# Optimization experiments

Hardware: AMD Instinct MI355X
Metric: run time of the kernel (lower is better)

## Reference

```python
import jax, jax.numpy as jnp
import numpy as np

HIDDEN = 256
EDGE_DIM = 16
HEADS = 8
HEAD_DIM = HIDDEN // HEADS
B, N = 4, 512


def setup_inputs() -> dict:
    key = jax.random.key(0)
    ks = jax.random.split(key, 16)
    s = 1.0 / np.sqrt(HIDDEN)
    se = 1.0 / np.sqrt(EDGE_DIM)
    return {
        "node_h": jax.random.normal(ks[0], (B, N, HIDDEN), jnp.float32),
        "edge_x": jax.random.normal(ks[1], (B, N, N, EDGE_DIM), jnp.float32),
        "edge_mask": jax.random.randint(ks[2], (B, N, N), 0, 2, jnp.int32),
        "Wq": jax.random.normal(ks[3], (HIDDEN, HIDDEN), jnp.float32) * s,
        "bq": jnp.zeros((HIDDEN,), jnp.float32),
        "Wk": jax.random.normal(ks[4], (HIDDEN, HIDDEN), jnp.float32) * s,
        "bk": jnp.zeros((HIDDEN,), jnp.float32),
        "Wv": jax.random.normal(ks[5], (HIDDEN, HIDDEN), jnp.float32) * s,
        "bv": jnp.zeros((HIDDEN,), jnp.float32),
        "We1": jax.random.normal(ks[6], (EDGE_DIM, HIDDEN), jnp.float32) * se,
        "be1": jnp.zeros((HIDDEN,), jnp.float32),
        "We2": jax.random.normal(ks[7], (HIDDEN, HEADS), jnp.float32) * s,
        "be2": jnp.zeros((HEADS,), jnp.float32),
        "Wo": jax.random.normal(ks[8], (HIDDEN, HIDDEN), jnp.float32) * s,
        "bo": jnp.zeros((HIDDEN,), jnp.float32),
        "ln_g": jnp.ones((HIDDEN,), jnp.float32),
        "ln_b": jnp.zeros((HIDDEN,), jnp.float32),
    }


def reference(node_h, edge_x, edge_mask, Wq, bq, Wk, bk, Wv, bv,
              We1, be1, We2, be2, Wo, bo, ln_g, ln_b):
    Bsz, Nn, _ = node_h.shape
    # projections -> [B, H, N, D]
    def heads(x):
        return x.reshape(Bsz, Nn, HEADS, HEAD_DIM).transpose(0, 2, 1, 3)
    q = heads(node_h @ Wq + bq)
    k = heads(node_h @ Wk + bk)
    v = heads(node_h @ Wv + bv)

    scores = jnp.einsum('bhid,bhjd->bhij', q, k) / np.sqrt(HEAD_DIM)
    scores = jax.nn.leaky_relu(scores, negative_slope=0.2)

    # edge bias MLP: [B,N,N,E] -> [B,N,N,H] -> [B,H,N,N]
    eb = jax.nn.relu(edge_x @ We1 + be1) @ We2 + be2
    scores = scores + eb.transpose(0, 3, 1, 2)

    valid = (edge_mask != 0) | jnp.eye(Nn, dtype=bool)[None]  # [B,N,N]
    scores = jnp.where(valid[:, None], scores, -1e9)

    attn = jax.nn.softmax(scores, axis=-1)
    out = jnp.einsum('bhij,bhjd->bhid', attn, v)
    out = out.transpose(0, 2, 1, 3).reshape(Bsz, Nn, HIDDEN)
    out = out @ Wo + bo

    x = node_h + out
    mu = jnp.mean(x, axis=-1, keepdims=True)
    var = jnp.var(x, axis=-1, keepdims=True)
    x = (x - mu) / jnp.sqrt(var + 1e-5) * ln_g + ln_b
    return jax.nn.relu(x), attn
```

## Files before the change

kernel.cpp:

```cpp
#include <hip/hip_runtime.h>

#define BATCH 4
#define NN 512
#define HID 256
#define EDIM 16
#define HEADS 8
#define HDIM 32

typedef __attribute__((ext_vector_type(8))) short bf16x8;
typedef __attribute__((ext_vector_type(4))) float f32x4;

__device__ inline unsigned short bf16_hi(float x){ return (unsigned short)(__float_as_uint(x)>>16); }
__device__ inline float bf16_f(unsigned short s){ return __uint_as_float(((unsigned)s)<<16); }
__device__ inline unsigned short bf16_rn(float x){
    unsigned u = __float_as_uint(x);
    unsigned r = u + 0x7FFFu + ((u>>16)&1u);
    return (unsigned short)(r>>16);
}
__device__ inline unsigned cvt_pk_bf16(float a, float b){
    unsigned d;
    asm("v_cvt_pk_bf16_f32 %0, %1, %2" : "=v"(d) : "v"(a), "v"(b));
    return d;
}
__device__ inline void hilo8(float4 A, float4 B, bf16x8& hi, bf16x8& lo){
    float xs[8] = {A.x,A.y,A.z,A.w,B.x,B.y,B.z,B.w};
    unsigned hu[4], lu[4];
#pragma unroll
    for (int p = 0; p < 4; ++p){
        unsigned u0 = __float_as_uint(xs[2*p]), u1 = __float_as_uint(xs[2*p+1]);
        float h0 = __uint_as_float(u0 & 0xFFFF0000u);
        float h1 = __uint_as_float(u1 & 0xFFFF0000u);
        hu[p] = (u0 >> 16) | (u1 & 0xFFFF0000u);
        lu[p] = cvt_pk_bf16(xs[2*p] - h0, xs[2*p+1] - h1);
    }
    int4 hv; hv.x = hu[0]; hv.y = hu[1]; hv.z = hu[2]; hv.w = hu[3];
    int4 lv; lv.x = lu[0]; lv.y = lu[1]; lv.z = lu[2]; lv.w = lu[3];
    hi = *(bf16x8*)&hv; lo = *(bf16x8*)&lv;
}

__global__ void k_pack(const float* __restrict__ We1, const float* __restrict__ be1,
                       const float* __restrict__ We2,
                       unsigned short* __restrict__ W1P, unsigned short* __restrict__ W2P) {
    int t = threadIdx.x;
#pragma unroll
    for (int rep = 0; rep < 4; ++rep) {
        int p = rep * 256 + t;
        int ut = p >> 6, lane = p & 63;
        int q = lane >> 4, r = lane & 15;
        int unit = ut * 16 + r;
#pragma unroll
        for (int j = 0; j < 8; ++j) {
            int k = q * 8 + j;
            unsigned short ov;
            if (k < 16) ov = bf16_hi(We1[k * HID + unit]);
            else if (k < 31) {
                float v = We1[(k - 16) * HID + unit];
                ov = bf16_rn(v - bf16_f(bf16_hi(v)));
            } else ov = bf16_rn(be1[unit]);
            W1P[p * 8 + j] = ov;
        }
    }
#pragma unroll
    for (int rep = 0; rep < 2; ++rep) {
        int p = rep * 256 + t;
        int kt = p >> 6, lane = p & 63;
        int q = lane >> 4, r = lane & 15;
#pragma unroll
        for (int jj = 0; jj < 8; ++jj) {
            int unit = kt * 32 + q * 8 + jj;
            W2P[p * 8 + jj] = (r < 8) ? bf16_rn(We2[unit * HEADS + r]) : (unsigned short)0;
        }
    }
}

__global__ __launch_bounds__(256) void k_qkv(
    const float* __restrict__ node_h,
    const float* __restrict__ Wq, const float* __restrict__ bq,
    const float* __restrict__ Wk, const float* __restrict__ bk,
    const float* __restrict__ Wv, const float* __restrict__ bv,
    float* __restrict__ q, float* __restrict__ k, float* __restrict__ vT) {
    int blk = blockIdx.x;
    int b = blk >> 7, i0 = (blk & 127) << 2;
    int t = threadIdx.x;
    __shared__ __align__(16) float s_h[4][HID];
#pragma unroll
    for (int u = 0; u < 4; ++u)
        s_h[u][t] = node_h[((size_t)b * NN + i0 + u) * HID + t];
    __syncthreads();
    float aq[4], ak[4], av[4];
    float bqv = bq[t], bkv = bk[t], bvv = bv[t];
#pragma unroll
    for (int u = 0; u < 4; ++u) { aq[u] = bqv; ak[u] = bkv; av[u] = bvv; }
#pragma unroll 4
    for (int rr = 0; rr < HID; ++rr) {
        float wq = Wq[rr * HID + t], wk = Wk[rr * HID + t], wv = Wv[rr * HID + t];
#pragma unroll
        for (int u = 0; u < 4; ++u) {
            float x = s_h[u][rr];
            aq[u] = fmaf(x, wq, aq[u]);
            ak[u] = fmaf(x, wk, ak[u]);
            av[u] = fmaf(x, wv, av[u]);
        }
    }
    int h = t >> 5, d = t & 31;
#pragma unroll
    for (int u = 0; u < 4; ++u) {
        size_t idx = ((size_t)(b * HEADS + h) * NN + i0 + u) * HDIM + d;
        q[idx] = aq[u]; k[idx] = ak[u];
        vT[((size_t)(b * HEADS + h) * HDIM + d) * NN + i0 + u] = av[u];
    }
}

__global__ __launch_bounds__(256, 3) void k_eb(
    const float* __restrict__ edge_x,
    const unsigned short* __restrict__ W1P, const unsigned short* __restrict__ W2P,
    const float* __restrict__ be2, float* __restrict__ eb) {
    int bid = blockIdx.x;
    int b = bid >> 9, i0 = ((bid >> 2) & 127) << 2, jq = bid & 3;
    int t = threadIdx.x;
    int w = t >> 6, lane = t & 63;
    int q2 = lane >> 4, r = lane & 15;

    __shared__ __align__(16) unsigned short sW1[8192];
    __shared__ __align__(16) unsigned short sW2[4096];

    {
        const float4* s1 = (const float4*)W1P;
        float4* d1 = (float4*)sW1;
#pragma unroll
        for (int rep = 0; rep < 4; ++rep) d1[rep * 256 + t] = s1[rep * 256 + t];
        const float4* s2 = (const float4*)W2P;
        float4* d2 = (float4*)sW2;
#pragma unroll
        for (int rep = 0; rep < 2; ++rep) d2[rep * 256 + t] = s2[rep * 256 + t];
    }
    __syncthreads();

    float be2r = (r < 8) ? be2[r] : 0.f;
    const char* wb1 = (const char*)sW1 + lane * 16;
    const char* wb2 = (const char*)sW2 + lane * 16;

    size_t xbase = (((size_t)b * NN + i0 + w) * NN) * EDIM + (size_t)((q2 & 1) * 8);
    const f32x4 zero4 = {0.f, 0.f, 0.f, 0.f};

    for (int sc = 0; sc < 2; ++sc) {
        int cc0 = jq * 8 + sc * 4;
        float4 xv[8];
#pragma unroll
        for (int x = 0; x < 4; ++x) {
            const float4* px = (const float4*)(edge_x + xbase + (size_t)((cc0 + x) * 16 + r) * EDIM);
            xv[2 * x]     = px[0];
            xv[2 * x + 1] = px[1];
        }
        bf16x8 bx[4];
#pragma unroll
        for (int x = 0; x < 4; ++x) {
            unsigned u0 = cvt_pk_bf16(xv[2*x].x, xv[2*x].y);
            unsigned u1 = cvt_pk_bf16(xv[2*x].z, xv[2*x].w);
            unsigned u2 = cvt_pk_bf16(xv[2*x+1].x, xv[2*x+1].y);
            unsigned u3 = cvt_pk_bf16(xv[2*x+1].z, xv[2*x+1].w);
            if (q2 == 3) u3 = (u3 & 0xFFFFu) | 0x3F800000u;
            int4 bxi; bxi.x = u0; bxi.y = u1; bxi.z = u2; bxi.w = u3;
            bx[x] = *(bf16x8*)&bxi;
        }
        f32x4 acc0[4], acc1[4];
#pragma unroll
        for (int x = 0; x < 4; ++x) {
            acc0[x] = (f32x4){be2r, be2r, be2r, be2r};
            acc1[x] = zero4;
        }
#pragma unroll
        for (int ktp = 0; ktp < 8; ++ktp) {
            bf16x8 wa = *(const bf16x8*)(wb1 + (2 * ktp) * 1024);
            bf16x8 wb = *(const bf16x8*)(wb1 + (2 * ktp + 1) * 1024);
            bf16x8 w2 = *(const bf16x8*)(wb2 + ktp * 1024);
#pragma unroll
            for (int x = 0; x < 4; ++x) {
                f32x4 c0 = __builtin_amdgcn_mfma_f32_16x16x32_bf16(wa, bx[x], zero4, 0, 0, 0);
                f32x4 c1 = __builtin_amdgcn_mfma_f32_16x16x32_bf16(wb, bx[x], zero4, 0, 0, 0);
                unsigned P0 = cvt_pk_bf16(fmaxf(c0[0], 0.f), fmaxf(c0[1], 0.f));
                unsigned P1 = cvt_pk_bf16(fmaxf(c0[2], 0.f), fmaxf(c0[3], 0.f));
                unsigned Q0 = cvt_pk_bf16(fmaxf(c1[0], 0.f), fmaxf(c1[1], 0.f));
                unsigned Q1 = cvt_pk_bf16(fmaxf(c1[2], 0.f), fmaxf(c1[3], 0.f));
                asm("v_permlane32_swap_b32 %0, %1" : "+v"(P0), "+v"(Q0));
                asm("v_permlane16_swap_b32 %0, %1" : "+v"(P0), "+v"(Q0));
                asm("v_permlane32_swap_b32 %0, %1" : "+v"(P1), "+v"(Q1));
                asm("v_permlane16_swap_b32 %0, %1" : "+v"(P1), "+v"(Q1));
                int4 ai; ai.x = (int)P0; ai.y = (int)P1; ai.z = (int)Q0; ai.w = (int)Q1;
                if (ktp & 1)
                    acc1[x] = __builtin_amdgcn_mfma_f32_16x16x32_bf16(*(bf16x8*)&ai, w2, acc1[x], 0, 0, 0);
                else
                    acc0[x] = __builtin_amdgcn_mfma_f32_16x16x32_bf16(*(bf16x8*)&ai, w2, acc0[x], 0, 0, 0);
            }
        }
        if (r < 8) {
#pragma unroll
            for (int x = 0; x < 4; ++x) {
                f32x4 a = acc0[x] + acc1[x];
                *(f32x4*)(eb + (((size_t)(b * HEADS + r) * NN) + (i0 + w)) * NN + (cc0 + x) * 16 + q2 * 4) = a;
            }
        }
    }
}

__global__ __launch_bounds__(256, 3) void k_attn2(
    const int* __restrict__ emask,
    const float* __restrict__ q, const float* __restrict__ k, const float* __restrict__ vT,
    float* attn, float* __restrict__ ao) {
    int bid = blockIdx.x;
    int b = bid >> 8, h = (bid >> 5) & 7, ic = bid & 31;
    int i0 = ic << 4;
    int t = threadIdx.x, w = t >> 6, lane = t & 63;
    int q2 = lane >> 4, r = lane & 15;
    size_t bh = (size_t)b * HEADS + h;

    __shared__ __align__(16) float s_sc[16][516];
    __shared__ __align__(16) unsigned short s_ab[16][520];
    __shared__ float s_out[2][16][33];

    bf16x8 qhi, qlo;
    {
        const float4* qp = (const float4*)(q + ((bh * NN) + i0 + r) * HDIM + q2 * 8);
        hilo8(qp[0], qp[1], qhi, qlo);
    }

    const float scale = 0.17677669529663687f;
    for (int c = 0; c < 8; ++c) {
        int jt = w * 8 + c;
        bf16x8 khi, klo;
        {
            const float4* kp = (const float4*)(k + (bh * NN + jt * 16 + r) * HDIM + q2 * 8);
            hilo8(kp[0], kp[1], khi, klo);
        }
        f32x4 cc = {0.f, 0.f, 0.f, 0.f};
        cc = __builtin_amdgcn_mfma_f32_16x16x32_bf16(qhi, khi, cc, 0, 0, 0);
        cc = __builtin_amdgcn_mfma_f32_16x16x32_bf16(qhi, klo, cc, 0, 0, 0);
        cc = __builtin_amdgcn_mfma_f32_16x16x32_bf16(qlo, khi, cc, 0, 0, 0);
        int j = jt * 16 + r;
#pragma unroll
        for (int reg = 0; reg < 4; ++reg) {
            int row = q2 * 4 + reg;
            int i = i0 + row;
            float s = cc[reg] * scale;
            s = s > 0.f ? s : 0.2f * s;
            s += attn[(bh * NN + i) * NN + j];
            bool valid = (emask[((size_t)b * NN + i) * NN + j] != 0) || (j == i);
            s_sc[row][j] = valid ? s : -1e9f;
        }
    }
    __syncthreads();

#pragma unroll
    for (int rr = 0; rr < 4; ++rr) {
        int row = w * 4 + rr;
        f32x4 v0 = *(f32x4*)&s_sc[row][lane * 8];
        f32x4 v1 = *(f32x4*)&s_sc[row][lane * 8 + 4];
        float mx = fmaxf(fmaxf(fmaxf(v0[0], v0[1]), fmaxf(v0[2], v0[3])),
                         fmaxf(fmaxf(v1[0], v1[1]), fmaxf(v1[2], v1[3])));
#pragma unroll
        for (int off = 32; off > 0; off >>= 1) mx = fmaxf(mx, __shfl_xor(mx, off));
        float e[8];
        e[0] = __expf(v0[0] - mx); e[1] = __expf(v0[1] - mx);
        e[2] = __expf(v0[2] - mx); e[3] = __expf(v0[3] - mx);
        e[4] = __expf(v1[0] - mx); e[5] = __expf(v1[1] - mx);
        e[6] = __expf(v1[2] - mx); e[7] = __expf(v1[3] - mx);
        float sum = ((e[0] + e[1]) + (e[2] + e[3])) + ((e[4] + e[5]) + (e[6] + e[7]));
#pragma unroll
        for (int off = 32; off > 0; off >>= 1) sum += __shfl_xor(sum, off);
        float inv = 1.f / sum;
#pragma unroll
        for (int l = 0; l < 8; ++l) e[l] *= inv;
        float* arow = attn + (bh * NN + i0 + row) * NN + lane * 8;
        float4 o0; o0.x = e[0]; o0.y = e[1]; o0.z = e[2]; o0.w = e[3];
        float4 o1; o1.x = e[4]; o1.y = e[5]; o1.z = e[6]; o1.w = e[7];
        *(float4*)(arow) = o0;
        *(float4*)(arow + 4) = o1;
        uint4 pk;
        pk.x = cvt_pk_bf16(e[0], e[1]); pk.y = cvt_pk_bf16(e[2], e[3]);
        pk.z = cvt_pk_bf16(e[4], e[5]); pk.w = cvt_pk_bf16(e[6], e[7]);
        *(uint4*)((char*)s_ab + row * 1040 + lane * 16) = pk;
    }
    __syncthreads();

    {
        int part = w >> 1, nh = w & 1;
        const float* vbase = vT + (bh * HDIM + nh * 16 + r) * NN;
        f32x4 acc = {0.f, 0.f, 0.f, 0.f};
        for (int kt = 0; kt < 16; ++kt) {
            bf16x8 af = *(bf16x8*)((char*)s_ab + r * 1040 + kt * 64 + q2 * 16);
            const float4* vp = (const float4*)(vbase + kt * 32 + q2 * 8);
            float4 x0 = vp[0], x1 = vp[1];
            float xs[8] = {x0.x, x0.y, x0.z, x0.w, x1.x, x1.y, x1.z, x1.w};
            bf16x8 bfg;
            if (part == 0) {
                unsigned hu[4];
#pragma unroll
                for (int p = 0; p < 4; ++p) {
                    unsigned a0 = __float_as_uint(xs[2*p]), a1 = __float_as_uint(xs[2*p+1]);
                    hu[p] = (a0 >> 16) | (a1 & 0xFFFF0000u);
                }
                int4 hv; hv.x = hu[0]; hv.y = hu[1]; hv.z = hu[2]; hv.w = hu[3];
                bfg = *(bf16x8*)&hv;
            } else {
                unsigned lu[4];
#pragma unroll
                for (int p = 0; p < 4; ++p) {
                    unsigned a0 = __float_as_uint(xs[2*p]), a1 = __float_as_uint(xs[2*p+1]);
                    float h0 = __uint_as_float(a0 & 0xFFFF0000u);
                    float h1 = __uint_as_float(a1 & 0xFFFF0000u);
                    lu[p] = cvt_pk_bf16(xs[2*p] - h0, xs[2*p+1] - h1);
                }
                int4 lv; lv.x = lu[0]; lv.y = lu[1]; lv.z = lu[2]; lv.w = lu[3];
                bfg = *(bf16x8*)&lv;
            }
            acc = __builtin_amdgcn_mfma_f32_16x16x32_bf16(af, bfg, acc, 0, 0, 0);
        }
#pragma unroll
        for (int reg = 0; reg < 4; ++reg)
            s_out[part][q2 * 4 + reg][nh * 16 + r] = acc[reg];
    }
    __syncthreads();

#pragma unroll
    for (int rep = 0; rep < 2; ++rep) {
        int idx = rep * 256 + t;
        int row = idx >> 5, d = idx & 31;
        ao[((size_t)b * NN + i0 + row) * HID + h * HDIM + d] =
            s_out[0][row][d] + s_out[1][row][d];
    }
}

__global__ __launch_bounds__(256) void k_final(
    const float* __restrict__ ao, const float* __restrict__ node_h,
    const float* __restrict__ Wo, const float* __restrict__ bo,
    const float* __restrict__ ln_g, const float* __restrict__ ln_b,
    float* __restrict__ out) {
    int blk = blockIdx.x;
    size_t bi0 = (size_t)blk * 4;
    int t = threadIdx.x;
    __shared__ __align__(16) float s_a[4][HID];
    __shared__ float s_red[4][4][2];
#pragma unroll
    for (int u = 0; u < 4; ++u)
        s_a[u][t] = ao[(bi0 + u) * HID + t];
    __syncthreads();
    float bov = bo[t];
    float o[4];
#pragma unroll
    for (int u = 0; u < 4; ++u) o[u] = bov;
#pragma unroll 4
    for (int rr = 0; rr < HID; ++rr) {
        float wo = Wo[rr * HID + t];
#pragma unroll
        for (int u = 0; u < 4; ++u) o[u] = fmaf(s_a[u][rr], wo, o[u]);
    }
    float g = ln_g[t], bb = ln_b[t];
    int wave = t >> 6, ln = t & 63;
    float x[4];
#pragma unroll
    for (int u = 0; u < 4; ++u) {
        x[u] = node_h[(bi0 + u) * HID + t] + o[u];
        float s1 = x[u], s2 = x[u] * x[u];
#pragma unroll
        for (int off = 32; off > 0; off >>= 1) { s1 += __shfl_xor(s1, off); s2 += __shfl_xor(s2, off); }
        if (ln == 0) { s_red[u][wave][0] = s1; s_red[u][wave][1] = s2; }
    }
    __syncthreads();
#pragma unroll
    for (int u = 0; u < 4; ++u) {
        float s1 = s_red[u][0][0] + s_red[u][1][0] + s_red[u][2][0] + s_red[u][3][0];
        float s2 = s_red[u][0][1] + s_red[u][1][1] + s_red[u][2][1] + s_red[u][3][1];
        float mean = s1 * (1.f / HID);
        float var = s2 * (1.f / HID) - mean * mean;
        float inv = rsqrtf(var + 1e-5f);
        float y = (x[u] - mean) * inv * g + bb;
        out[(bi0 + u) * HID + t] = fmaxf(y, 0.f);
    }
}

extern "C" void kernel_launch(void* const* d_in, const int* in_sizes, int n_in,
                              void* d_out, int out_size, void* d_ws, size_t ws_size,
                              hipStream_t stream) {
    const float* node_h = (const float*)d_in[0];
    const float* edge_x = (const float*)d_in[1];
    const int*   emask  = (const int*)d_in[2];
    const float* Wq = (const float*)d_in[3];
    const float* bq = (const float*)d_in[4];
    const float* Wk = (const float*)d_in[5];
    const float* bk = (const float*)d_in[6];
    const float* Wv = (const float*)d_in[7];
    const float* bv = (const float*)d_in[8];
    const float* We1 = (const float*)d_in[9];
    const float* be1 = (const float*)d_in[10];
    const float* We2 = (const float*)d_in[11];
    const float* be2 = (const float*)d_in[12];
    const float* Wo = (const float*)d_in[13];
    const float* bo = (const float*)d_in[14];
    const float* ln_g = (const float*)d_in[15];
    const float* ln_b = (const float*)d_in[16];

    float* out_x  = (float*)d_out;
    float* out_at = (float*)d_out + (size_t)BATCH * NN * HID;

    float* ws = (float*)d_ws;
    float* q    = ws;
    float* kbuf = ws + 524288;
    float* vT   = ws + 1048576;
    float* ao   = ws + 1572864;
    unsigned short* W1P = (unsigned short*)(ws + 2097152);
    unsigned short* W2P = W1P + 8192;

    const int NBI = BATCH * NN;

    hipLaunchKernelGGL(k_pack, dim3(1), dim3(256), 0, stream, We1, be1, We2, W1P, W2P);
    hipLaunchKernelGGL(k_qkv, dim3(NBI / 4), dim3(256), 0, stream,
                       node_h, Wq, bq, Wk, bk, Wv, bv, q, kbuf, vT);
    hipLaunchKernelGGL(k_eb, dim3(2048), dim3(256), 0, stream,
                       edge_x, W1P, W2P, be2, out_at);
    hipLaunchKernelGGL(k_attn2, dim3(1024), dim3(256), 0, stream,
                       emask, q, kbuf, vT, out_at, ao);
    hipLaunchKernelGGL(k_final, dim3(NBI / 4), dim3(256), 0, stream,
                       ao, node_h, Wo, bo, ln_g, ln_b, out_x);
}
```

Baseline: 147.6 us.

## Precompute bf16 hi/lo splits of K and V in projection kernel

The QKV projection kernel now writes K and V as separate bf16 hi and lo arrays, so the attention kernel no longer converts fp32 to bf16 in its inner loops. The attention kernel loads the bf16 fragments directly, which halves K/V read traffic per MFMA pass and drops the V conversion ALU work. It also reuses the score shared-memory buffer for the packed probabilities and raises the occupancy hint from 3 to 4 blocks. The cost is extra scattered 2-byte stores in k_qkv, and the aliasing of s_sc relies on the barrier between the softmax and PV phases.

Result: faster. 138.9 us (-5.9%).

```diff
diff --git a/kernel.cpp b/kernel.cpp
--- a/kernel.cpp
+++ b/kernel.cpp
@@ -78,7 +78,9 @@
     const float* __restrict__ Wq, const float* __restrict__ bq,
     const float* __restrict__ Wk, const float* __restrict__ bk,
     const float* __restrict__ Wv, const float* __restrict__ bv,
-    float* __restrict__ q, float* __restrict__ k, float* __restrict__ vT) {
+    float* __restrict__ q,
+    unsigned short* __restrict__ khi, unsigned short* __restrict__ klo,
+    unsigned short* __restrict__ vhi, unsigned short* __restrict__ vlo) {
     int blk = blockIdx.x;
     int b = blk >> 7, i0 = (blk & 127) << 2;
     int t = threadIdx.x;
@@ -106,8 +108,14 @@
 #pragma unroll
     for (int u = 0; u < 4; ++u) {
         size_t idx = ((size_t)(b * HEADS + h) * NN + i0 + u) * HDIM + d;
-        q[idx] = aq[u]; k[idx] = ak[u];
-        vT[((size_t)(b * HEADS + h) * HDIM + d) * NN + i0 + u] = av[u];
+        q[idx] = aq[u];
+        unsigned short kh = bf16_hi(ak[u]);
+        khi[idx] = kh;
+        klo[idx] = bf16_rn(ak[u] - bf16_f(kh));
+        size_t vidx = ((size_t)(b * HEADS + h) * HDIM + d) * NN + i0 + u;
+        unsigned short vh = bf16_hi(av[u]);
+        vhi[vidx] = vh;
+        vlo[vidx] = bf16_rn(av[u] - bf16_f(vh));
     }
 }
 
@@ -203,9 +211,10 @@
     }
 }
 
-__global__ __launch_bounds__(256, 3) void k_attn2(
-    const int* __restrict__ emask,
-    const float* __restrict__ q, const float* __restrict__ k, const float* __restrict__ vT,
+__global__ __launch_bounds__(256, 4) void k_attn2(
+    const int* __restrict__ emask, const float* __restrict__ q,
+    const unsigned short* __restrict__ khi, const unsigned short* __restrict__ klo,
+    const unsigned short* __restrict__ vhi, const unsigned short* __restrict__ vlo,
     float* attn, float* __restrict__ ao) {
     int bid = blockIdx.x;
     int b = bid >> 8, h = (bid >> 5) & 7, ic = bid & 31;
@@ -215,8 +224,8 @@
     size_t bh = (size_t)b * HEADS + h;
 
     __shared__ __align__(16) float s_sc[16][516];
-    __shared__ __align__(16) unsigned short s_ab[16][520];
     __shared__ float s_out[2][16][33];
+    char* sab = (char*)&s_sc[0][0];
 
     bf16x8 qhi, qlo;
     {
@@ -227,15 +236,13 @@
     const float scale = 0.17677669529663687f;
     for (int c = 0; c < 8; ++c) {
         int jt = w * 8 + c;
-        bf16x8 khi, klo;
-        {
-            const float4* kp = (const float4*)(k + (bh * NN + jt * 16 + r) * HDIM + q2 * 8);
-            hilo8(kp[0], kp[1], khi, klo);
-        }
+        size_t kidx = (bh * NN + jt * 16 + r) * HDIM + q2 * 8;
+        bf16x8 kh8 = *(const bf16x8*)(khi + kidx);
+        bf16x8 kl8 = *(const bf16x8*)(klo + kidx);
         f32x4 cc = {0.f, 0.f, 0.f, 0.f};
-        cc = __builtin_amdgcn_mfma_f32_16x16x32_bf16(qhi, khi, cc, 0, 0, 0);
-        cc = __builtin_amdgcn_mfma_f32_16x16x32_bf16(qhi, klo, cc, 0, 0, 0);
-        cc = __builtin_amdgcn_mfma_f32_16x16x32_bf16(qlo, khi, cc, 0, 0, 0);
+        cc = __builtin_amdgcn_mfma_f32_16x16x32_bf16(qhi, kh8, cc, 0, 0, 0);
+        cc = __builtin_amdgcn_mfma_f32_16x16x32_bf16(qhi, kl8, cc, 0, 0, 0);
+        cc = __builtin_amdgcn_mfma_f32_16x16x32_bf16(qlo, kh8, cc, 0, 0, 0);
         int j = jt * 16 + r;
 #pragma unroll
         for (int reg = 0; reg < 4; ++reg) {
@@ -278,41 +285,17 @@
         uint4 pk;
         pk.x = cvt_pk_bf16(e[0], e[1]); pk.y = cvt_pk_bf16(e[2], e[3]);
         pk.z = cvt_pk_bf16(e[4], e[5]); pk.w = cvt_pk_bf16(e[6], e[7]);
-        *(uint4*)((char*)s_ab + row * 1040 + lane * 16) = pk;
+        *(uint4*)(sab + row * 2064 + lane * 16) = pk;
     }
     __syncthreads();
 
     {
         int part = w >> 1, nh = w & 1;
-        const float* vbase = vT + (bh * HDIM + nh * 16 + r) * NN;
+        const unsigned short* vbase = (part == 0 ? vhi : vlo) + (bh * HDIM + nh * 16 + r) * NN;
         f32x4 acc = {0.f, 0.f, 0.f, 0.f};
         for (int kt = 0; kt < 16; ++kt) {
-            bf16x8 af = *(bf16x8*)((char*)s_ab + r * 1040 + kt * 64 + q2 * 16);
-            const float4* vp = (const float4*)(vbase + kt * 32 + q2 * 8);
-            float4 x0 = vp[0], x1 = vp[1];
-            float xs[8] = {x0.x, x0.y, x0.z, x0.w, x1.x, x1.y, x1.z, x1.w};
-            bf16x8 bfg;
-            if (part == 0) {
-                unsigned hu[4];
-#pragma unroll
-                for (int p = 0; p < 4; ++p) {
-                    unsigned a0 = __float_as_uint(xs[2*p]), a1 = __float_as_uint(xs[2*p+1]);
-                    hu[p] = (a0 >> 16) | (a1 & 0xFFFF0000u);
-                }
-                int4 hv; hv.x = hu[0]; hv.y = hu[1]; hv.z = hu[2]; hv.w = hu[3];
-                bfg = *(bf16x8*)&hv;
-            } else {
-                unsigned lu[4];
-#pragma unroll
-                for (int p = 0; p < 4; ++p) {
-                    unsigned a0 = __float_as_uint(xs[2*p]), a1 = __float_as_uint(xs[2*p+1]);
-                    float h0 = __uint_as_float(a0 & 0xFFFF0000u);
-                    float h1 = __uint_as_float(a1 & 0xFFFF0000u);
-                    lu[p] = cvt_pk_bf16(xs[2*p] - h0, xs[2*p+1] - h1);
-                }
-                int4 lv; lv.x = lu[0]; lv.y = lu[1]; lv.z = lu[2]; lv.w = lu[3];
-                bfg = *(bf16x8*)&lv;
-            }
+            bf16x8 af = *(bf16x8*)(sab + r * 2064 + kt * 64 + q2 * 16);
+            bf16x8 bfg = *(const bf16x8*)(vbase + kt * 32 + q2 * 8);
             acc = __builtin_amdgcn_mfma_f32_16x16x32_bf16(af, bfg, acc, 0, 0, 0);
         }
 #pragma unroll
@@ -403,22 +386,24 @@
     float* out_at = (float*)d_out + (size_t)BATCH * NN * HID;
 
     float* ws = (float*)d_ws;
-    float* q    = ws;
-    float* kbuf = ws + 524288;
-    float* vT   = ws + 1048576;
-    float* ao   = ws + 1572864;
-    unsigned short* W1P = (unsigned short*)(ws + 2097152);
+    float* q = ws;
+    unsigned short* khi = (unsigned short*)(ws + 524288);
+    unsigned short* klo = khi + 524288;
+    unsigned short* vhi = klo + 524288;
+    unsigned short* vlo = vhi + 524288;
+    float* ao = (float*)(vlo + 524288);
+    unsigned short* W1P = (unsigned short*)(ao + 524288);
     unsigned short* W2P = W1P + 8192;
 
     const int NBI = BATCH * NN;
 
     hipLaunchKernelGGL(k_pack, dim3(1), dim3(256), 0, stream, We1, be1, We2, W1P, W2P);
     hipLaunchKernelGGL(k_qkv, dim3(NBI / 4), dim3(256), 0, stream,
-                       node_h, Wq, bq, Wk, bk, Wv, bv, q, kbuf, vT);
+                       node_h, Wq, bq, Wk, bk, Wv, bv, q, khi, klo, vhi, vlo);
     hipLaunchKernelGGL(k_eb, dim3(2048), dim3(256), 0, stream,
                        edge_x, W1P, W2P, be2, out_at);
     hipLaunchKernelGGL(k_attn2, dim3(1024), dim3(256), 0, stream,
-                       emask, q, kbuf, vT, out_at, ao);
+                       emask, q, khi, klo, vhi, vlo, out_at, ao);
     hipLaunchKernelGGL(k_final, dim3(NBI / 4), dim3(256), 0, stream,
                        ao, node_h, Wo, bo, ln_g, ln_b, out_x);
 }
```
